# Optimization experiments

Measured on AMD Instinct MI355X. Metric: run time of the kernel, lower is better.

Reference implementation:

```python
import jax, jax.numpy as jnp
import numpy as np

BATCH, DIM, M, T = 256, 256, 64, 256
NUM_ITERS = 4
ZERO_HEAD = 16  # first 16 entries of U are zero (unweighted low-freq coeffs)


def setup_inputs() -> dict:
    key = jax.random.key(0)
    k1, k2, k3 = jax.random.split(key, 3)
    y = jax.random.normal(k1, (BATCH, DIM, T), dtype=jnp.float32)
    # small-norm measurement matrix so spectral radius of S stays < 1
    A = 0.02 * jax.random.normal(k2, (M, DIM), dtype=jnp.float32)
    # near-identity dictionary (trained D stays well-conditioned)
    D = jnp.eye(DIM, dtype=jnp.float32) + 0.02 * jax.random.normal(k3, (DIM, DIM), dtype=jnp.float32)
    F = jnp.eye(DIM, dtype=jnp.float32)
    lam1 = jnp.float32(0.5)
    lam2 = jnp.float32(1.0)
    alpha = jnp.float32(1.0)
    h0 = jnp.zeros((DIM,), dtype=jnp.float32)
    U = jnp.ones((DIM,), dtype=jnp.float32).at[:ZERO_HEAD].set(0.0)
    return {"y": y, "A": A, "D": D, "F": F, "lam1": lam1, "lam2": lam2,
            "alpha": alpha, "h0": h0, "U": U}


def _soft_threshold(z, U, b):
    # sign(z) * relu(|z| - U*b)
    return jnp.sign(z) * jnp.maximum(jnp.abs(z) - U * b, 0.0)


def reference(y, A, D, F, lam1, lam2, alpha, h0, U):
    dim = D.shape[0]
    I = jnp.eye(dim, dtype=D.dtype)
    P = D.T @ F @ D                                      # (dim, dim)
    S = I - (1.0 / alpha) * (D.T @ (A.T @ A + lam2 * I) @ D)  # (dim, dim)
    V = (1.0 / alpha) * (D.T @ A.T)                      # (dim, m)
    x = jnp.einsum('md,bdt->tbm', A, y)                  # measurements, (T, B, m)
    b = lam1 / alpha
    c2 = lam2 / alpha

    def step(h_pre, x_t):
        # h_pre: (B, dim), x_t: (B, m)
        Ph = h_pre @ P.T                                 # (B, dim)
        const = x_t @ V.T + c2 * Ph                      # (B, dim), fixed over inner iters
        h_t = Ph
        for _ in range(NUM_ITERS):
            h_t = _soft_threshold(h_t @ S.T + const, U, b)
        return h_t, h_t

    h_init = jnp.broadcast_to(h0, (y.shape[0], dim))
    _, hs = jax.lax.scan(step, h_init, x)                # hs: (T, B, dim)
    h = jnp.transpose(hs, (1, 2, 0))                     # (B, dim, T)
    return jnp.einsum('nd,bdt->bnt', D, h)               # y_re: (B, dim, T)
```

## Files before the change

### kernel.cpp

```cpp
#include <hip/hip_runtime.h>
#include <hip/hip_bf16.h>

typedef unsigned int u32;
typedef unsigned short u16;

#define DIMN 256
#define TLEN 256

typedef _Float16 half2v __attribute__((ext_vector_type(2)));
typedef _Float16 f16x8  __attribute__((ext_vector_type(8)));
typedef float    f32x4  __attribute__((ext_vector_type(4)));

__device__ __forceinline__ u32 packh2(float lo, float hi) {
    _Float16 l = (_Float16)lo, h = (_Float16)hi;
    u16 lu = __builtin_bit_cast(u16, l);
    u16 hu = __builtin_bit_cast(u16, h);
    return (u32)lu | ((u32)hu << 16);
}

__device__ __forceinline__ float h2lo(u32 v) {
    return (float)__builtin_bit_cast(half2v, v).x;
}
__device__ __forceinline__ float h2hi(u32 v) {
    return (float)__builtin_bit_cast(half2v, v).y;
}

__global__ void prep1(const float* __restrict__ A, const float* __restrict__ D,
                      const float* __restrict__ F, const float* __restrict__ lam2p,
                      float* __restrict__ FD, float* __restrict__ G,
                      float* __restrict__ AD) {
    int gid = blockIdx.x * 256 + threadIdx.x;
    if (gid < 65536) {
        int k = gid >> 8, j = gid & 255;
        float s = 0.f;
        #pragma unroll 8
        for (int q = 0; q < 256; ++q) s += F[k*256+q] * D[q*256+j];
        FD[gid] = s;
    } else if (gid < 131072) {
        int g = gid - 65536; int p = g >> 8, q = g & 255;
        float s = (p == q) ? lam2p[0] : 0.f;
        #pragma unroll 8
        for (int m = 0; m < 64; ++m) s += A[m*256+p] * A[m*256+q];
        G[g] = s;
    } else if (gid < 147456) {
        int g = gid - 131072; int m = g >> 8, i = g & 255;
        float s = 0.f;
        #pragma unroll 8
        for (int k = 0; k < 256; ++k) s += A[m*256+k] * D[k*256+i];
        AD[g] = s;
    }
}

__global__ void prep2(const float* __restrict__ A, const float* __restrict__ D,
                      const float* __restrict__ alphap,
                      const float* __restrict__ FD, const float* __restrict__ G,
                      const float* __restrict__ AD,
                      float* __restrict__ Pt, float* __restrict__ GD,
                      float* __restrict__ Wt) {
    int gid = blockIdx.x * 256 + threadIdx.x;
    float inva = 1.0f / alphap[0];
    if (gid < 65536) {
        int j = gid >> 8, i = gid & 255;
        float s = 0.f;
        #pragma unroll 8
        for (int k = 0; k < 256; ++k) s += D[k*256+i] * FD[k*256+j];
        Pt[gid] = s;
    } else if (gid < 131072) {
        int g = gid - 65536; int k = g >> 8, j = g & 255;
        float s = 0.f;
        #pragma unroll 8
        for (int q = 0; q < 256; ++q) s += G[k*256+q] * D[q*256+j];
        GD[g] = s;
    } else {
        int g = gid - 131072; int d = g >> 8, i = g & 255;
        float s = 0.f;
        #pragma unroll 8
        for (int m = 0; m < 64; ++m) s += AD[m*256+i] * A[m*256+d];
        Wt[g] = inva * s;
    }
}

__global__ void prep3(const float* __restrict__ D, const float* __restrict__ GD,
                      const float* __restrict__ alphap, float* __restrict__ St) {
    int gid = blockIdx.x * 256 + threadIdx.x;
    int j = gid >> 8, i = gid & 255;
    float inva = 1.0f / alphap[0];
    float s = 0.f;
    #pragma unroll 8
    for (int k = 0; k < 256; ++k) s += D[k*256+i] * GD[k*256+j];
    St[gid] = ((i == j) ? 1.0f : 0.0f) - inva * s;
}

__global__ void prep5(const float* __restrict__ St, const float* __restrict__ Pt,
                      const float* __restrict__ lam2p, const float* __restrict__ alphap,
                      float* __restrict__ Qt) {
    int gid = blockIdx.x * 256 + threadIdx.x;
    int j = gid >> 8, i = gid & 255;
    float c2 = lam2p[0] / alphap[0];
    float s = c2 * Pt[j*256 + i];
    #pragma unroll 8
    for (int k = 0; k < 256; ++k) s += St[k*256+i] * Pt[j*256+k];
    Qt[gid] = s;
}

__global__ void prep4(const float* __restrict__ St, const float* __restrict__ Pt,
                      const float* __restrict__ Qt,
                      u32* __restrict__ Sfrag, u32* __restrict__ Pfrag,
                      u32* __restrict__ Qfrag) {
    int gid = blockIdx.x * 256 + threadIdx.x;
    int sel = gid >> 13;
    int idx = gid & 8191;
    int l   = idx & 63;
    int kk  = (idx >> 6) & 7;
    int tau = idx >> 9;
    int row = 16*tau + (l & 15);
    int k0  = 32*kk + 8*(l >> 4);
    const float* M = (sel == 0) ? St : (sel == 1) ? Pt : Qt;
    u32* O = (sel == 0) ? Sfrag : (sel == 1) ? Pfrag : Qfrag;
    uint4 v;
    v.x = packh2(M[(k0+0)*256 + row], M[(k0+1)*256 + row]);
    v.y = packh2(M[(k0+2)*256 + row], M[(k0+3)*256 + row]);
    v.z = packh2(M[(k0+4)*256 + row], M[(k0+5)*256 + row]);
    v.w = packh2(M[(k0+6)*256 + row], M[(k0+7)*256 + row]);
    *(uint4*)&O[idx*4] = v;
}

__launch_bounds__(256, 2)
__global__ void zgemm(const float* __restrict__ y, const float* __restrict__ Wt,
                      u32* __restrict__ Zh) {
    __shared__ float ys[64][132];
    __shared__ float wsh[64][132];
    const int b  = blockIdx.x;
    const int t0 = (blockIdx.y & 1) * 128;
    const int i0 = (blockIdx.y >> 1) * 128;
    const int tid = threadIdx.x;
    const int tx = tid & 15;
    const int ty = tid >> 4;
    float acc[8][8];
    #pragma unroll
    for (int c = 0; c < 8; ++c)
        #pragma unroll
        for (int a = 0; a < 8; ++a) acc[c][a] = 0.f;

    for (int dc = 0; dc < 256; dc += 64) {
        #pragma unroll
        for (int k = 0; k < 8; ++k) {
            int idx = k * 256 + tid;
            int row = idx >> 5, col4 = idx & 31;
            float4 yv = *(const float4*)&y[((size_t)b*256 + dc + row)*256 + t0 + col4*4];
            float4 wv = *(const float4*)&Wt[(size_t)(dc + row)*256 + i0 + col4*4];
            *(float4*)&ys[row][col4*4]  = yv;
            *(float4*)&wsh[row][col4*4] = wv;
        }
        __syncthreads();
        #pragma unroll 4
        for (int dd = 0; dd < 64; ++dd) {
            float4 w0 = *(const float4*)&wsh[dd][8*tx];
            float4 w1 = *(const float4*)&wsh[dd][8*tx+4];
            float4 y0 = *(const float4*)&ys[dd][8*ty];
            float4 y1 = *(const float4*)&ys[dd][8*ty+4];
            float wv[8] = {w0.x,w0.y,w0.z,w0.w,w1.x,w1.y,w1.z,w1.w};
            float yv[8] = {y0.x,y0.y,y0.z,y0.w,y1.x,y1.y,y1.z,y1.w};
            #pragma unroll
            for (int c = 0; c < 8; ++c)
                #pragma unroll
                for (int a = 0; a < 8; ++a) acc[c][a] += wv[a] * yv[c];
        }
        __syncthreads();
    }
    #pragma unroll
    for (int c = 0; c < 8; ++c) {
        int t = t0 + 8*ty + c;
        uint4 pk;
        pk.x = packh2(acc[c][0], acc[c][1]);
        pk.y = packh2(acc[c][2], acc[c][3]);
        pk.z = packh2(acc[c][4], acc[c][5]);
        pk.w = packh2(acc[c][6], acc[c][7]);
        *(uint4*)&Zh[((size_t)b*256 + t)*128 + (i0 >> 1) + 4*tx] = pk;
    }
}

__global__ __attribute__((amdgpu_flat_work_group_size(512, 512),
                          amdgpu_waves_per_eu(2, 2)))
void scan9(const u32* __restrict__ Sfrag, const u32* __restrict__ Pfrag,
           const u32* __restrict__ Qfrag,
           const u32* __restrict__ Zh,
           const float* __restrict__ h0, const float* __restrict__ U,
           const float* __restrict__ lam1p, const float* __restrict__ lam2p,
           const float* __restrict__ alphap,
           float* __restrict__ H) {
    __shared__ __align__(16) u32 hx[2 * 2048];

    const int tid = threadIdx.x;
    const int l   = tid & 63;
    const int w   = tid >> 6;
    const int lb  = l & 15;
    const int g   = l >> 4;
    const int b   = blockIdx.x * 16 + lb;

    const float inva = 1.0f / alphap[0];
    const float bt   = lam1p[0] * inva;
    const float c2   = lam2p[0] * inva;

    const int rb = 32*w + 4*g;
    const float u00 = U[rb+0]*bt,  u01 = U[rb+1]*bt,  u02 = U[rb+2]*bt,  u03 = U[rb+3]*bt;
    const float u10 = U[rb+16]*bt, u11 = U[rb+17]*bt, u12 = U[rb+18]*bt, u13 = U[rb+19]*bt;

    f16x8 Sf0[8], Sf1[8], Pf0[8], Pf1[8], Qf0[8], Qf1[8];
    #pragma unroll
    for (int kk = 0; kk < 8; ++kk) {
        Sf0[kk] = __builtin_bit_cast(f16x8, *(const uint4*)&Sfrag[(((2*w+0)*8 + kk)*64 + l)*4]);
        Sf1[kk] = __builtin_bit_cast(f16x8, *(const uint4*)&Sfrag[(((2*w+1)*8 + kk)*64 + l)*4]);
        Pf0[kk] = __builtin_bit_cast(f16x8, *(const uint4*)&Pfrag[(((2*w+0)*8 + kk)*64 + l)*4]);
        Pf1[kk] = __builtin_bit_cast(f16x8, *(const uint4*)&Pfrag[(((2*w+1)*8 + kk)*64 + l)*4]);
        Qf0[kk] = __builtin_bit_cast(f16x8, *(const uint4*)&Qfrag[(((2*w+0)*8 + kk)*64 + l)*4]);
        Qf1[kk] = __builtin_bit_cast(f16x8, *(const uint4*)&Qfrag[(((2*w+1)*8 + kk)*64 + l)*4]);
    }

    {
        int k0 = 32*(tid >> 6) + 8*((tid & 63) >> 4);
        uint4 hv;
        hv.x = packh2(h0[k0+0], h0[k0+1]);
        hv.y = packh2(h0[k0+2], h0[k0+3]);
        hv.z = packh2(h0[k0+4], h0[k0+5]);
        hv.w = packh2(h0[k0+6], h0[k0+7]);
        *(uint4*)&hx[tid*4] = hv;
    }
    __syncthreads();

    const u32* Zb = Zh + (size_t)b*32768 + 16*w + 2*g;
    float* Hb = H + (size_t)b*TLEN*DIMN + 32*w + 4*g;

    const int wb0 = w*256 + (((g>>1))*16 + lb)*4 + (g&1)*2;

    uint2 z0 = *(const uint2*)&Zb[0];
    uint2 z1 = *(const uint2*)&Zb[8];

    #pragma unroll 1
    for (int t = 0; t < TLEN; ++t) {
        f16x8 hb[8];
        #pragma unroll
        for (int kk = 0; kk < 8; ++kk)
            hb[kk] = __builtin_bit_cast(f16x8, *(const uint4*)&hx[0 + (kk*64 + l)*4]);
        f32x4 q0 = {h2lo(z0.x), h2hi(z0.x), h2lo(z0.y), h2hi(z0.y)};
        f32x4 q1 = {h2lo(z1.x), h2hi(z1.x), h2lo(z1.y), h2hi(z1.y)};
        f32x4 a0 = {0.f,0.f,0.f,0.f}, a1 = {0.f,0.f,0.f,0.f};
        #pragma unroll
        for (int kk = 0; kk < 8; ++kk) {
            q0 = __builtin_amdgcn_mfma_f32_16x16x32_f16(Qf0[kk], hb[kk], q0, 0, 0, 0);
            q1 = __builtin_amdgcn_mfma_f32_16x16x32_f16(Qf1[kk], hb[kk], q1, 0, 0, 0);
            a0 = __builtin_amdgcn_mfma_f32_16x16x32_f16(Pf0[kk], hb[kk], a0, 0, 0, 0);
            a1 = __builtin_amdgcn_mfma_f32_16x16x32_f16(Pf1[kk], hb[kk], a1, 0, 0, 0);
        }
        {
            const float h00 = copysignf(fmaxf(fabsf(q0[0]) - u00, 0.f), q0[0]);
            const float h01 = copysignf(fmaxf(fabsf(q0[1]) - u01, 0.f), q0[1]);
            const float h02 = copysignf(fmaxf(fabsf(q0[2]) - u02, 0.f), q0[2]);
            const float h03 = copysignf(fmaxf(fabsf(q0[3]) - u03, 0.f), q0[3]);
            const float h10 = copysignf(fmaxf(fabsf(q1[0]) - u10, 0.f), q1[0]);
            const float h11 = copysignf(fmaxf(fabsf(q1[1]) - u11, 0.f), q1[1]);
            const float h12 = copysignf(fmaxf(fabsf(q1[2]) - u12, 0.f), q1[2]);
            const float h13 = copysignf(fmaxf(fabsf(q1[3]) - u13, 0.f), q1[3]);
            *(uint2*)&hx[2048 + wb0]       = make_uint2(packh2(h00,h01), packh2(h02,h03));
            *(uint2*)&hx[2048 + wb0 + 128] = make_uint2(packh2(h10,h11), packh2(h12,h13));
        }
        __syncthreads();

        const int tn = (t < TLEN-1) ? t + 1 : t;
        uint2 zn0 = *(const uint2*)&Zb[(size_t)tn*128];
        uint2 zn1 = *(const uint2*)&Zb[(size_t)tn*128 + 8];

        const float c00 = h2lo(z0.x) + c2*a0[0];
        const float c01 = h2hi(z0.x) + c2*a0[1];
        const float c02 = h2lo(z0.y) + c2*a0[2];
        const float c03 = h2hi(z0.y) + c2*a0[3];
        const float c10 = h2lo(z1.x) + c2*a1[0];
        const float c11 = h2hi(z1.x) + c2*a1[1];
        const float c12 = h2lo(z1.y) + c2*a1[2];
        const float c13 = h2hi(z1.y) + c2*a1[3];

        #pragma unroll
        for (int it = 0; it < 3; ++it) {
            const int rd = (it & 1) ? 0 : 2048;
            const int wr = (it & 1) ? 2048 : 0;
            #pragma unroll
            for (int kk = 0; kk < 8; ++kk)
                hb[kk] = __builtin_bit_cast(f16x8, *(const uint4*)&hx[rd + (kk*64 + l)*4]);
            f32x4 s0 = {c00,c01,c02,c03};
            f32x4 s1 = {c10,c11,c12,c13};
            #pragma unroll
            for (int kk = 0; kk < 8; ++kk) {
                s0 = __builtin_amdgcn_mfma_f32_16x16x32_f16(Sf0[kk], hb[kk], s0, 0, 0, 0);
                s1 = __builtin_amdgcn_mfma_f32_16x16x32_f16(Sf1[kk], hb[kk], s1, 0, 0, 0);
            }
            const float h00 = copysignf(fmaxf(fabsf(s0[0]) - u00, 0.f), s0[0]);
            const float h01 = copysignf(fmaxf(fabsf(s0[1]) - u01, 0.f), s0[1]);
            const float h02 = copysignf(fmaxf(fabsf(s0[2]) - u02, 0.f), s0[2]);
            const float h03 = copysignf(fmaxf(fabsf(s0[3]) - u03, 0.f), s0[3]);
            const float h10 = copysignf(fmaxf(fabsf(s1[0]) - u10, 0.f), s1[0]);
            const float h11 = copysignf(fmaxf(fabsf(s1[1]) - u11, 0.f), s1[1]);
            const float h12 = copysignf(fmaxf(fabsf(s1[2]) - u12, 0.f), s1[2]);
            const float h13 = copysignf(fmaxf(fabsf(s1[3]) - u13, 0.f), s1[3]);
            *(uint2*)&hx[wr + wb0]       = make_uint2(packh2(h00,h01), packh2(h02,h03));
            *(uint2*)&hx[wr + wb0 + 128] = make_uint2(packh2(h10,h11), packh2(h12,h13));
            __syncthreads();
            if (it == 2) {
                *(float4*)&Hb[(size_t)t*DIMN]      = make_float4(h00, h01, h02, h03);
                *(float4*)&Hb[(size_t)t*DIMN + 16] = make_float4(h10, h11, h12, h13);
            }
        }
        z0 = zn0; z1 = zn1;
    }
}

__launch_bounds__(256, 2)
__global__ void ogemm(const float* __restrict__ D, const float* __restrict__ H,
                      float* __restrict__ out) {
    __shared__ float Ds[64][132];
    __shared__ float Hs[64][132];
    const int b  = blockIdx.x;
    const int n0 = (blockIdx.y & 1) * 128;
    const int t0 = (blockIdx.y >> 1) * 128;
    const int tid = threadIdx.x;
    const int tx = tid & 15;
    const int ty = tid >> 4;
    float acc[8][8];
    #pragma unroll
    for (int a = 0; a < 8; ++a)
        #pragma unroll
        for (int c = 0; c < 8; ++c) acc[a][c] = 0.f;

    for (int dc = 0; dc < 256; dc += 64) {
        #pragma unroll
        for (int k = 0; k < 8; ++k) {
            int idx = k * 256 + tid;
            int row = idx >> 4;
            int d4  = idx & 15;
            float4 dv = *(const float4*)&D[((size_t)(n0 + row))*256 + dc + d4*4];
            float4 hv = *(const float4*)&H[((size_t)b*256 + t0 + row)*256 + dc + d4*4];
            Ds[d4*4+0][row] = dv.x; Ds[d4*4+1][row] = dv.y;
            Ds[d4*4+2][row] = dv.z; Ds[d4*4+3][row] = dv.w;
            Hs[d4*4+0][row] = hv.x; Hs[d4*4+1][row] = hv.y;
            Hs[d4*4+2][row] = hv.z; Hs[d4*4+3][row] = hv.w;
        }
        __syncthreads();
        #pragma unroll 4
        for (int dd = 0; dd < 64; ++dd) {
            float4 d0 = *(const float4*)&Ds[dd][8*tx];
            float4 d1 = *(const float4*)&Ds[dd][8*tx+4];
            float4 h0v = *(const float4*)&Hs[dd][8*ty];
            float4 h1v = *(const float4*)&Hs[dd][8*ty+4];
            float dv[8] = {d0.x,d0.y,d0.z,d0.w,d1.x,d1.y,d1.z,d1.w};
            float hv[8] = {h0v.x,h0v.y,h0v.z,h0v.w,h1v.x,h1v.y,h1v.z,h1v.w};
            #pragma unroll
            for (int a = 0; a < 8; ++a)
                #pragma unroll
                for (int c = 0; c < 8; ++c) acc[a][c] += dv[a] * hv[c];
        }
        __syncthreads();
    }
    #pragma unroll
    for (int a = 0; a < 8; ++a) {
        float* op = &out[((size_t)b*256 + n0 + 8*tx + a)*256 + t0 + 8*ty];
        *(float4*)(op)     = make_float4(acc[a][0], acc[a][1], acc[a][2], acc[a][3]);
        *(float4*)(op + 4) = make_float4(acc[a][4], acc[a][5], acc[a][6], acc[a][7]);
    }
}

extern "C" void kernel_launch(void* const* d_in, const int* in_sizes, int n_in,
                              void* d_out, int out_size, void* d_ws, size_t ws_size,
                              hipStream_t stream) {
    const float* y     = (const float*)d_in[0];
    const float* A     = (const float*)d_in[1];
    const float* D     = (const float*)d_in[2];
    const float* F     = (const float*)d_in[3];
    const float* lam1  = (const float*)d_in[4];
    const float* lam2  = (const float*)d_in[5];
    const float* alpha = (const float*)d_in[6];
    const float* h0    = (const float*)d_in[7];
    const float* U     = (const float*)d_in[8];
    float* out = (float*)d_out;
    float* ws  = (float*)d_ws;

    const size_t oZ  = 0;
    const size_t oH  = 16777216;
    const size_t oWt = 33554432;
    const size_t oSt = 33619968;
    const size_t oPt = 33685504;
    const size_t oFD = 33751040;
    const size_t oG  = 33816576;
    const size_t oGD = 33882112;
    const size_t oAD = 33947648;
    const size_t oSh = 33964032;
    const size_t oPh = 33996800;

    u32*   Zh = (u32*)(ws + oZ);
    float* H  = ws + oH;
    float* Wt = ws + oWt; float* St = ws + oSt; float* Pt = ws + oPt;
    float* FD = ws + oFD; float* G  = ws + oG;  float* GD = ws + oGD;
    float* AD = ws + oAD;
    float* Qt = ws + oFD;
    u32* Sfrag = (u32*)(ws + oSh);
    u32* Pfrag = (u32*)(ws + oPh);
    u32* Qfrag = (u32*)(ws + oG);

    prep1<<<576, 256, 0, stream>>>(A, D, F, lam2, FD, G, AD);
    prep2<<<768, 256, 0, stream>>>(A, D, alpha, FD, G, AD, Pt, GD, Wt);
    prep3<<<256, 256, 0, stream>>>(D, GD, alpha, St);
    prep5<<<256, 256, 0, stream>>>(St, Pt, lam2, alpha, Qt);
    prep4<<<96, 256, 0, stream>>>(St, Pt, Qt, Sfrag, Pfrag, Qfrag);
    {
        dim3 g(256, 4);
        zgemm<<<g, 256, 0, stream>>>(y, Wt, Zh);
    }
    scan9<<<16, 512, 0, stream>>>(Sfrag, Pfrag, Qfrag, Zh, h0, U, lam1, lam2, alpha, H);
    {
        dim3 g(256, 4);
        ogemm<<<g, 256, 0, stream>>>(D, H, out);
    }
}
```

Before: 950.5 us.

## Move input and output GEMMs to fp16 MFMA and store H in fp16

Replaces the fp32 FMA-based zgemm and ogemm with MFMA 16x16x32 fp16 kernels. The W and D weights are pre-packed into fragment layout by prep kernels, and y or H tiles are staged in swizzled LDS. The scan now writes H as packed fp16, which halves its write and read traffic. This targets the compute and bandwidth cost of the two large batched GEMMs. The trade-off is extra fp16 rounding of y and H, plus an output store pattern that writes scalar strided elements instead of float4.

Measured after the change: 789.6 us. -16.9%, faster.

```diff
diff --git a/kernel.cpp b/kernel.cpp
--- a/kernel.cpp
+++ b/kernel.cpp
@@ -104,9 +104,9 @@
 }
 
 __global__ void prep4(const float* __restrict__ St, const float* __restrict__ Pt,
-                      const float* __restrict__ Qt,
+                      const float* __restrict__ Qt, const float* __restrict__ Wt,
                       u32* __restrict__ Sfrag, u32* __restrict__ Pfrag,
-                      u32* __restrict__ Qfrag) {
+                      u32* __restrict__ Qfrag, u32* __restrict__ Wfrag) {
     int gid = blockIdx.x * 256 + threadIdx.x;
     int sel = gid >> 13;
     int idx = gid & 8191;
@@ -115,8 +115,8 @@
     int tau = idx >> 9;
     int row = 16*tau + (l & 15);
     int k0  = 32*kk + 8*(l >> 4);
-    const float* M = (sel == 0) ? St : (sel == 1) ? Pt : Qt;
-    u32* O = (sel == 0) ? Sfrag : (sel == 1) ? Pfrag : Qfrag;
+    const float* M = (sel == 0) ? St : (sel == 1) ? Pt : (sel == 2) ? Qt : Wt;
+    u32* O = (sel == 0) ? Sfrag : (sel == 1) ? Pfrag : (sel == 2) ? Qfrag : Wfrag;
     uint4 v;
     v.x = packh2(M[(k0+0)*256 + row], M[(k0+1)*256 + row]);
     v.y = packh2(M[(k0+2)*256 + row], M[(k0+3)*256 + row]);
@@ -125,58 +125,90 @@
     *(uint4*)&O[idx*4] = v;
 }
 
-__launch_bounds__(256, 2)
-__global__ void zgemm(const float* __restrict__ y, const float* __restrict__ Wt,
-                      u32* __restrict__ Zh) {
-    __shared__ float ys[64][132];
-    __shared__ float wsh[64][132];
-    const int b  = blockIdx.x;
-    const int t0 = (blockIdx.y & 1) * 128;
-    const int i0 = (blockIdx.y >> 1) * 128;
+__global__ void prep6(const float* __restrict__ D, u32* __restrict__ Dfrag) {
+    int idx = blockIdx.x * 256 + threadIdx.x;
+    int l   = idx & 63;
+    int kk  = (idx >> 6) & 7;
+    int tau = idx >> 9;
+    int row = 16*tau + (l & 15);
+    int k0  = 32*kk + 8*(l >> 4);
+    float4 fa = *(const float4*)&D[row*256 + k0];
+    float4 fb = *(const float4*)&D[row*256 + k0 + 4];
+    uint4 v;
+    v.x = packh2(fa.x, fa.y);
+    v.y = packh2(fa.z, fa.w);
+    v.z = packh2(fb.x, fb.y);
+    v.w = packh2(fb.z, fb.w);
+    *(uint4*)&Dfrag[idx*4] = v;
+}
+
+__global__ __attribute__((amdgpu_flat_work_group_size(512, 512),
+                          amdgpu_waves_per_eu(2)))
+void zgemm2(const float* __restrict__ y, const u32* __restrict__ Wfrag,
+            u32* __restrict__ Zh) {
+    __shared__ u32 yl[16384];
     const int tid = threadIdx.x;
-    const int tx = tid & 15;
-    const int ty = tid >> 4;
-    float acc[8][8];
-    #pragma unroll
-    for (int c = 0; c < 8; ++c)
-        #pragma unroll
-        for (int a = 0; a < 8; ++a) acc[c][a] = 0.f;
-
-    for (int dc = 0; dc < 256; dc += 64) {
-        #pragma unroll
-        for (int k = 0; k < 8; ++k) {
-            int idx = k * 256 + tid;
-            int row = idx >> 5, col4 = idx & 31;
-            float4 yv = *(const float4*)&y[((size_t)b*256 + dc + row)*256 + t0 + col4*4];
-            float4 wv = *(const float4*)&Wt[(size_t)(dc + row)*256 + i0 + col4*4];
-            *(float4*)&ys[row][col4*4]  = yv;
-            *(float4*)&wsh[row][col4*4] = wv;
-        }
-        __syncthreads();
-        #pragma unroll 4
-        for (int dd = 0; dd < 64; ++dd) {
-            float4 w0 = *(const float4*)&wsh[dd][8*tx];
-            float4 w1 = *(const float4*)&wsh[dd][8*tx+4];
-            float4 y0 = *(const float4*)&ys[dd][8*ty];
-            float4 y1 = *(const float4*)&ys[dd][8*ty+4];
-            float wv[8] = {w0.x,w0.y,w0.z,w0.w,w1.x,w1.y,w1.z,w1.w};
-            float yv[8] = {y0.x,y0.y,y0.z,y0.w,y1.x,y1.y,y1.z,y1.w};
-            #pragma unroll
-            for (int c = 0; c < 8; ++c)
-                #pragma unroll
-                for (int a = 0; a < 8; ++a) acc[c][a] += wv[a] * yv[c];
-        }
-        __syncthreads();
-    }
-    #pragma unroll
-    for (int c = 0; c < 8; ++c) {
-        int t = t0 + 8*ty + c;
-        uint4 pk;
-        pk.x = packh2(acc[c][0], acc[c][1]);
-        pk.y = packh2(acc[c][2], acc[c][3]);
-        pk.z = packh2(acc[c][4], acc[c][5]);
-        pk.w = packh2(acc[c][6], acc[c][7]);
-        *(uint4*)&Zh[((size_t)b*256 + t)*128 + (i0 >> 1) + 4*tx] = pk;
+    const int l   = tid & 63;
+    const int w   = tid >> 6;
+    const int g   = l >> 4;
+    const int c   = l & 15;
+    const int b   = blockIdx.x;
+    const int t0  = blockIdx.y * 128;
+
+    #pragma unroll
+    for (int it = 0; it < 8; ++it) {
+        int idx = it * 512 + tid;
+        int dp = idx >> 5;
+        int tq = idx & 31;
+        const float* yb = y + ((size_t)b*256 + 2*dp)*256 + t0 + 4*tq;
+        float4 fa = *(const float4*)yb;
+        float4 fb = *(const float4*)(yb + 256);
+        const float* fav = (const float*)&fa;
+        const float* fbv = (const float*)&fb;
+        #pragma unroll
+        for (int j = 0; j < 4; ++j) {
+            int tl = 4*tq + j;
+            yl[tl*128 + (dp ^ ((tl & 7) << 2))] = packh2(fav[j], fbv[j]);
+        }
+    }
+
+    f16x8 Wf0[8], Wf1[8];
+    #pragma unroll
+    for (int kk = 0; kk < 8; ++kk) {
+        Wf0[kk] = __builtin_bit_cast(f16x8, *(const uint4*)&Wfrag[(((2*w+0)*8 + kk)*64 + l)*4]);
+        Wf1[kk] = __builtin_bit_cast(f16x8, *(const uint4*)&Wfrag[(((2*w+1)*8 + kk)*64 + l)*4]);
+    }
+    __syncthreads();
+
+    f32x4 acc0[8], acc1[8];
+    #pragma unroll
+    for (int tt = 0; tt < 8; ++tt) {
+        acc0[tt] = (f32x4){0.f,0.f,0.f,0.f};
+        acc1[tt] = (f32x4){0.f,0.f,0.f,0.f};
+    }
+    const int swz = (c & 7) << 2;
+    #pragma unroll
+    for (int tt = 0; tt < 8; ++tt) {
+        const int tl = 16*tt + c;
+        #pragma unroll
+        for (int kk = 0; kk < 8; ++kk) {
+            int idx = tl*128 + ((16*kk + 4*g) ^ swz);
+            f16x8 bf = __builtin_bit_cast(f16x8, *(const uint4*)&yl[idx]);
+            acc0[tt] = __builtin_amdgcn_mfma_f32_16x16x32_f16(Wf0[kk], bf, acc0[tt], 0, 0, 0);
+            acc1[tt] = __builtin_amdgcn_mfma_f32_16x16x32_f16(Wf1[kk], bf, acc1[tt], 0, 0, 0);
+        }
+    }
+    #pragma unroll
+    for (int tt = 0; tt < 8; ++tt) {
+        const int t = t0 + 16*tt + c;
+        uint2 p0, p1;
+        p0.x = packh2(acc0[tt][0], acc0[tt][1]);
+        p0.y = packh2(acc0[tt][2], acc0[tt][3]);
+        p1.x = packh2(acc1[tt][0], acc1[tt][1]);
+        p1.y = packh2(acc1[tt][2], acc1[tt][3]);
+        u32* zp = &Zh[((size_t)(b*256 + t))*128 + 16*w + 2*g];
+        *(uint2*)(zp)     = p0;
+        *(uint2*)(zp + 8) = p1;
     }
 }
 
@@ -188,7 +220,7 @@
            const float* __restrict__ h0, const float* __restrict__ U,
            const float* __restrict__ lam1p, const float* __restrict__ lam2p,
            const float* __restrict__ alphap,
-           float* __restrict__ H) {
+           u32* __restrict__ Hh) {
     __shared__ __align__(16) u32 hx[2 * 2048];
 
     const int tid = threadIdx.x;
@@ -229,7 +261,7 @@
     __syncthreads();
 
     const u32* Zb = Zh + (size_t)b*32768 + 16*w + 2*g;
-    float* Hb = H + (size_t)b*TLEN*DIMN + 32*w + 4*g;
+    u32* Hbh = Hh + (size_t)b*32768 + 16*w + 2*g;
 
     const int wb0 = w*256 + (((g>>1))*16 + lb)*4 + (g&1)*2;
 
@@ -305,65 +337,71 @@
             *(uint2*)&hx[wr + wb0 + 128] = make_uint2(packh2(h10,h11), packh2(h12,h13));
             __syncthreads();
             if (it == 2) {
-                *(float4*)&Hb[(size_t)t*DIMN]      = make_float4(h00, h01, h02, h03);
-                *(float4*)&Hb[(size_t)t*DIMN + 16] = make_float4(h10, h11, h12, h13);
+                *(uint2*)&Hbh[(size_t)t*128]     = make_uint2(packh2(h00,h01), packh2(h02,h03));
+                *(uint2*)&Hbh[(size_t)t*128 + 8] = make_uint2(packh2(h10,h11), packh2(h12,h13));
             }
         }
         z0 = zn0; z1 = zn1;
     }
 }
 
-__launch_bounds__(256, 2)
-__global__ void ogemm(const float* __restrict__ D, const float* __restrict__ H,
-                      float* __restrict__ out) {
-    __shared__ float Ds[64][132];
-    __shared__ float Hs[64][132];
-    const int b  = blockIdx.x;
-    const int n0 = (blockIdx.y & 1) * 128;
-    const int t0 = (blockIdx.y >> 1) * 128;
+__global__ __attribute__((amdgpu_flat_work_group_size(512, 512),
+                          amdgpu_waves_per_eu(2)))
+void ogemm2(const u32* __restrict__ Dfrag, const u32* __restrict__ Hh,
+            float* __restrict__ out) {
+    __shared__ u32 hl[16384];
     const int tid = threadIdx.x;
-    const int tx = tid & 15;
-    const int ty = tid >> 4;
-    float acc[8][8];
-    #pragma unroll
-    for (int a = 0; a < 8; ++a)
-        #pragma unroll
-        for (int c = 0; c < 8; ++c) acc[a][c] = 0.f;
-
-    for (int dc = 0; dc < 256; dc += 64) {
-        #pragma unroll
-        for (int k = 0; k < 8; ++k) {
-            int idx = k * 256 + tid;
-            int row = idx >> 4;
-            int d4  = idx & 15;
-            float4 dv = *(const float4*)&D[((size_t)(n0 + row))*256 + dc + d4*4];
-            float4 hv = *(const float4*)&H[((size_t)b*256 + t0 + row)*256 + dc + d4*4];
-            Ds[d4*4+0][row] = dv.x; Ds[d4*4+1][row] = dv.y;
-            Ds[d4*4+2][row] = dv.z; Ds[d4*4+3][row] = dv.w;
-            Hs[d4*4+0][row] = hv.x; Hs[d4*4+1][row] = hv.y;
-            Hs[d4*4+2][row] = hv.z; Hs[d4*4+3][row] = hv.w;
-        }
-        __syncthreads();
-        #pragma unroll 4
-        for (int dd = 0; dd < 64; ++dd) {
-            float4 d0 = *(const float4*)&Ds[dd][8*tx];
-            float4 d1 = *(const float4*)&Ds[dd][8*tx+4];
-            float4 h0v = *(const float4*)&Hs[dd][8*ty];
-            float4 h1v = *(const float4*)&Hs[dd][8*ty+4];
-            float dv[8] = {d0.x,d0.y,d0.z,d0.w,d1.x,d1.y,d1.z,d1.w};
-            float hv[8] = {h0v.x,h0v.y,h0v.z,h0v.w,h1v.x,h1v.y,h1v.z,h1v.w};
-            #pragma unroll
-            for (int a = 0; a < 8; ++a)
-                #pragma unroll
-                for (int c = 0; c < 8; ++c) acc[a][c] += dv[a] * hv[c];
-        }
-        __syncthreads();
-    }
-    #pragma unroll
-    for (int a = 0; a < 8; ++a) {
-        float* op = &out[((size_t)b*256 + n0 + 8*tx + a)*256 + t0 + 8*ty];
-        *(float4*)(op)     = make_float4(acc[a][0], acc[a][1], acc[a][2], acc[a][3]);
-        *(float4*)(op + 4) = make_float4(acc[a][4], acc[a][5], acc[a][6], acc[a][7]);
+    const int l   = tid & 63;
+    const int w   = tid >> 6;
+    const int g   = l >> 4;
+    const int c   = l & 15;
+    const int b   = blockIdx.x;
+    const int t0  = blockIdx.y * 128;
+
+    const uint4* Hg = (const uint4*)(Hh + (size_t)b*32768 + (size_t)t0*128);
+    #pragma unroll
+    for (int it = 0; it < 8; ++it) {
+        int j4 = it * 512 + tid;
+        int tl = j4 >> 5, m = j4 & 31;
+        ((uint4*)hl)[tl*32 + (m ^ (tl & 7))] = Hg[j4];
+    }
+
+    f16x8 Df0[8], Df1[8];
+    #pragma unroll
+    for (int kk = 0; kk < 8; ++kk) {
+        Df0[kk] = __builtin_bit_cast(f16x8, *(const uint4*)&Dfrag[(((2*w+0)*8 + kk)*64 + l)*4]);
+        Df1[kk] = __builtin_bit_cast(f16x8, *(const uint4*)&Dfrag[(((2*w+1)*8 + kk)*64 + l)*4]);
+    }
+    __syncthreads();
+
+    f32x4 acc0[8], acc1[8];
+    #pragma unroll
+    for (int tt = 0; tt < 8; ++tt) {
+        acc0[tt] = (f32x4){0.f,0.f,0.f,0.f};
+        acc1[tt] = (f32x4){0.f,0.f,0.f,0.f};
+    }
+    const int swz = (c & 7) << 2;
+    #pragma unroll
+    for (int tt = 0; tt < 8; ++tt) {
+        const int tl = 16*tt + c;
+        #pragma unroll
+        for (int kk = 0; kk < 8; ++kk) {
+            int idx = tl*128 + ((16*kk + 4*g) ^ swz);
+            f16x8 bf = __builtin_bit_cast(f16x8, *(const uint4*)&hl[idx]);
+            acc0[tt] = __builtin_amdgcn_mfma_f32_16x16x32_f16(Df0[kk], bf, acc0[tt], 0, 0, 0);
+            acc1[tt] = __builtin_amdgcn_mfma_f32_16x16x32_f16(Df1[kk], bf, acc1[tt], 0, 0, 0);
+        }
+    }
+    #pragma unroll
+    for (int tt = 0; tt < 8; ++tt) {
+        const int t = t0 + 16*tt + c;
+        const int n0 = 16*(2*w+0) + 4*g;
+        const int n1 = 16*(2*w+1) + 4*g;
+        #pragma unroll
+        for (int r = 0; r < 4; ++r) {
+            out[((size_t)(b*256) + n0 + r)*256 + t] = acc0[tt][r];
+            out[((size_t)(b*256) + n1 + r)*256 + t] = acc1[tt][r];
+        }
     }
 }
 
@@ -395,7 +433,7 @@
     const size_t oPh = 33996800;
 
     u32*   Zh = (u32*)(ws + oZ);
-    float* H  = ws + oH;
+    u32*   Hh = (u32*)(ws + oH);
     float* Wt = ws + oWt; float* St = ws + oSt; float* Pt = ws + oPt;
     float* FD = ws + oFD; float* G  = ws + oG;  float* GD = ws + oGD;
     float* AD = ws + oAD;
@@ -403,19 +441,22 @@
     u32* Sfrag = (u32*)(ws + oSh);
     u32* Pfrag = (u32*)(ws + oPh);
     u32* Qfrag = (u32*)(ws + oG);
+    u32* Wfrag = (u32*)(ws + oGD);
+    u32* Dfrag = (u32*)(ws + oGD + 32768);
 
     prep1<<<576, 256, 0, stream>>>(A, D, F, lam2, FD, G, AD);
     prep2<<<768, 256, 0, stream>>>(A, D, alpha, FD, G, AD, Pt, GD, Wt);
     prep3<<<256, 256, 0, stream>>>(D, GD, alpha, St);
     prep5<<<256, 256, 0, stream>>>(St, Pt, lam2, alpha, Qt);
-    prep4<<<96, 256, 0, stream>>>(St, Pt, Qt, Sfrag, Pfrag, Qfrag);
+    prep4<<<128, 256, 0, stream>>>(St, Pt, Qt, Wt, Sfrag, Pfrag, Qfrag, Wfrag);
+    prep6<<<32, 256, 0, stream>>>(D, Dfrag);
     {
-        dim3 g(256, 4);
-        zgemm<<<g, 256, 0, stream>>>(y, Wt, Zh);
-    }
-    scan9<<<16, 512, 0, stream>>>(Sfrag, Pfrag, Qfrag, Zh, h0, U, lam1, lam2, alpha, H);
+        dim3 gz(256, 2);
+        zgemm2<<<gz, 512, 0, stream>>>(y, Wfrag, Zh);
+    }
+    scan9<<<16, 512, 0, stream>>>(Sfrag, Pfrag, Qfrag, Zh, h0, U, lam1, lam2, alpha, Hh);
     {
-        dim3 g(256, 4);
-        ogemm<<<g, 256, 0, stream>>>(D, H, out);
-    }
-}
+        dim3 go(256, 2);
+        ogemm2<<<go, 512, 0, stream>>>(Dfrag, Hh, out);
+    }
+}
```
